# Kernel optimization log

Measured on AMD Instinct MI355X. Metric: run time of the kernel, lower is better.

The kernel has to match this reference:

```python
import jax, jax.numpy as jnp
import numpy as np

B, N, FIN = 32, 1024, 6
KCHEB = 3
CLASS_NUM = 40


def _pairwise_adj(x):
    # x: [B, N, D] -> exp(-squared_euclidean_dist) adjacency [B, N, N]
    inner = jnp.einsum('bnd,bmd->bnm', x, x)
    sq = jnp.sum(x * x, axis=-1)
    d2 = sq[:, :, None] - 2.0 * inner + sq[:, None, :]
    return jnp.exp(-d2)


def _get_laplacian(adj):
    # normalized Laplacian: I - D^{-1/2} A D^{-1/2}
    deg = jnp.sum(adj, axis=-1)                       # [B, N]
    d_is = 1.0 / jnp.sqrt(deg)                        # [B, N]
    eye = jnp.eye(adj.shape[-1], dtype=adj.dtype)
    return eye - d_is[:, :, None] * adj * d_is[:, None, :]


def _cheb_conv(x, L, W, b):
    # Chebyshev graph conv: sum_k T_k(L) x W_k + b;  W: [K, Fin, Fout]
    x0 = x
    x1 = jnp.einsum('bnm,bmf->bnf', L, x0)
    out = jnp.einsum('bnf,fg->bng', x0, W[0]) + jnp.einsum('bnf,fg->bng', x1, W[1])
    xk_2, xk_1 = x0, x1
    for k in range(2, W.shape[0]):
        xk = 2.0 * jnp.einsum('bnm,bmf->bnf', L, xk_1) - xk_2
        out = out + jnp.einsum('bnf,fg->bng', xk, W[k])
        xk_2, xk_1 = xk_1, xk
    return out + b


def setup_inputs() -> dict:
    key = jax.random.key(0)
    ks = jax.random.split(key, 16)

    def w(k, shape, fan_in):
        return jax.random.normal(k, shape, dtype=jnp.float32) / np.sqrt(fan_in)

    return {
        'x': jax.random.normal(ks[0], (B, N, FIN), dtype=jnp.float32),
        'W1': w(ks[1], (KCHEB, 6, 128), 6 * KCHEB),
        'b1': jnp.zeros((128,), jnp.float32),
        'W2': w(ks[2], (KCHEB, 128, 512), 128 * KCHEB),
        'b2': jnp.zeros((512,), jnp.float32),
        'W3': w(ks[3], (KCHEB, 512, 1024), 512 * KCHEB),
        'b3': jnp.zeros((1024,), jnp.float32),
        'fc1_w': w(ks[4], (1024, 512), 1024),
        'fc1_b': jnp.zeros((512,), jnp.float32),
        'fc2_w': w(ks[5], (512, 128), 512),
        'fc2_b': jnp.zeros((128,), jnp.float32),
        'fc3_w': w(ks[6], (128, CLASS_NUM), 128),
        'fc3_b': jnp.zeros((CLASS_NUM,), jnp.float32),
    }


def reference(x, W1, b1, W2, b2, W3, b3, fc1_w, fc1_b, fc2_w, fc2_b, fc3_w, fc3_b):
    # Laplacians are computed under torch.no_grad in the original
    L = _get_laplacian(_pairwise_adj(x))
    out = jax.nn.relu(_cheb_conv(x, L, W1, b1))        # [B, N, 128]

    L = _get_laplacian(_pairwise_adj(out))
    out = jax.nn.relu(_cheb_conv(out, L, W2, b2))      # [B, N, 512]

    L = _get_laplacian(_pairwise_adj(out))
    out = jax.nn.relu(_cheb_conv(out, L, W3, b3))      # [B, N, 1024]

    out = jnp.max(out, axis=1)                          # global max pool -> [B, 1024]
    out = jax.nn.relu(out @ fc1_w + fc1_b)              # dropout is identity at eval
    out = jax.nn.relu(out @ fc2_w + fc2_b)
    out = out @ fc3_w + fc3_b                           # [B, CLASS_NUM]
    return out
```

## Files before the change

kernel.cpp:

```cpp
#include <hip/hip_runtime.h>
#include <cstddef>


#define NN 1024

typedef unsigned short ushort_t;
typedef __bf16 bf16x8 __attribute__((ext_vector_type(8)));
typedef float f32x4 __attribute__((ext_vector_type(4)));

__device__ inline ushort_t f2bf(float f) {
    unsigned int u = __float_as_uint(f);
    u = (u + 0x7fffu + ((u >> 16) & 1u)) >> 16;
    return (ushort_t)u;
}
__device__ inline float bf2f(ushort_t s) {
    return __uint_as_float(((unsigned int)s) << 16);
}

__device__ __attribute__((always_inline)) inline void gld16(
    const ushort_t* g, ushort_t* l) {
    __builtin_amdgcn_global_load_lds(
        (__attribute__((address_space(1))) void*)(ushort_t*)g,
        (__attribute__((address_space(3))) void*)l, 16, 0, 0);
}

__global__ void zero_kernel(float* __restrict__ p, int n) {
    int i = blockIdx.x * blockDim.x + threadIdx.x;
    if (i < n) p[i] = 0.f;
}

__global__ __launch_bounds__(256) void wconvT_kernel(
    const float* __restrict__ W, ushort_t* __restrict__ Wt, int Fi, int Fo, int Ks) {
    int p = blockIdx.z;
    int k0 = blockIdx.y * 64, g0 = blockIdx.x * 64;
    __shared__ float T[64][65];
    int t = threadIdx.x;
#pragma unroll
    for (int q = 0; q < 16; ++q) {
        int kr = (t >> 6) + 4 * q, gc = t & 63;
        int k = k0 + kr, g = g0 + gc;
        T[kr][gc] = (k < Fi && g < Fo) ? W[((size_t)p * Fi + k) * Fo + g] : 0.f;
    }
    __syncthreads();
#pragma unroll
    for (int q = 0; q < 16; ++q) {
        int gr = (t >> 6) + 4 * q, kc = t & 63;
        int g = g0 + gr, k = k0 + kc;
        if (g < Fo && k < Ks)
            Wt[((size_t)p * Fo + g) * Ks + k] = f2bf(T[kc][gr]);
    }
}

__global__ __launch_bounds__(256) void prep2_kernel(
    const float* __restrict__ X, ushort_t* __restrict__ hi, ushort_t* __restrict__ lo,
    ushort_t* __restrict__ Xt, float* __restrict__ sq, int F, int Fp, int bsh) {
    int L = blockIdx.x;
    int b = L & ((1 << bsh) - 1), n0 = (L >> bsh) * 64;
    int t = threadIdx.x;
    __shared__ float T[64][65];
    __shared__ float red[4][64];
    const float* Xb = X + ((size_t)b * NN + n0) * F;
    float sacc = 0.f;

    for (int f0 = 0; f0 < Fp; f0 += 64) {
        __syncthreads();
#pragma unroll
        for (int p = 0; p < 16; ++p) {
            int nr = (t >> 6) + 4 * p, fc = t & 63;
            int f = f0 + fc;
            T[nr][fc] = (f < F) ? Xb[(size_t)nr * F + f] : 0.f;
        }
        __syncthreads();
#pragma unroll
        for (int p = 0; p < 16; ++p) {
            int nr = (t >> 6) + 4 * p, fc = t & 63;
            int f = f0 + fc;
            if (f < Fp) {
                float x = T[nr][fc];
                ushort_t h = f2bf(x);
                size_t off = ((size_t)b * NN + n0 + nr) * Fp + f;
                hi[off] = h;
                lo[off] = f2bf(x - bf2f(h));
            }
        }
#pragma unroll
        for (int p = 0; p < 16; ++p) {
            int fr = (t >> 6) + 4 * p;
            int f = f0 + fr;
            if (f < F)
                Xt[((size_t)b * Fp + f) * NN + n0 + (t & 63)] = f2bf(T[t & 63][fr]);
        }
        {
            int nl = t & 63, fq = t >> 6;
#pragma unroll
            for (int fc = 0; fc < 16; ++fc) {
                float v = T[nl][fq * 16 + fc];
                sacc += v * v;
            }
        }
    }
    red[t >> 6][t & 63] = sacc;
    __syncthreads();
    if (t < 64)
        sq[(size_t)b * NN + n0 + t] = red[0][t] + red[1][t] + red[2][t] + red[3][t];
}

__global__ __launch_bounds__(256) void adj_kernel(
    const ushort_t* __restrict__ hi, const ushort_t* __restrict__ lo,
    const float* __restrict__ sq, ushort_t* __restrict__ Abf,
    float* __restrict__ deg_part, int Fp, int bsh, int BCv) {
    int t = threadIdx.x;
    int L = blockIdx.x;
    int b = L & ((1 << bsh) - 1);
    int rest = L >> bsh;
    int m0 = (rest & 7) * 128, n0 = (rest >> 3) * 128;
    const ushort_t* Hb = hi + (size_t)b * NN * Fp;
    const ushort_t* Lb = lo + (size_t)b * NN * Fp;
    ushort_t* Ab = Abf + (size_t)b * NN * NN;
    const float* sqb = sq + (size_t)b * NN;

    int lane = t & 63, quad = lane >> 4, l16 = lane & 15, wave = t >> 6;
    int rowoff = (wave >> 1) * 64, coloff = (wave & 1) * 64;

    __shared__ __align__(16) ushort_t smem[40960];

    f32x4 acc[4][4];
#pragma unroll
    for (int i = 0; i < 4; ++i)
#pragma unroll
        for (int j = 0; j < 4; ++j) acc[i][j] = (f32x4){0.f, 0.f, 0.f, 0.f};

    int rr0 = t >> 2, kq = (t & 3) * 8;
    int rr1 = rr0 + 64;
    const ushort_t* pAh0 = Hb + (size_t)(n0 + rr0) * Fp + kq;
    const ushort_t* pAh1 = Hb + (size_t)(n0 + rr1) * Fp + kq;
    const ushort_t* pAl0 = Lb + (size_t)(n0 + rr0) * Fp + kq;
    const ushort_t* pAl1 = Lb + (size_t)(n0 + rr1) * Fp + kq;
    const ushort_t* pBh0 = Hb + (size_t)(m0 + rr0) * Fp + kq;
    const ushort_t* pBh1 = Hb + (size_t)(m0 + rr1) * Fp + kq;
    const ushort_t* pBl0 = Lb + (size_t)(m0 + rr0) * Fp + kq;
    const ushort_t* pBl1 = Lb + (size_t)(m0 + rr1) * Fp + kq;
    int o0 = rr0 * 40 + kq, o1 = rr1 * 40 + kq;

    {
        *(uint4*)&smem[o0]         = *(const uint4*)pAh0;
        *(uint4*)&smem[o1]         = *(const uint4*)pAh1;
        *(uint4*)&smem[5120 + o0]  = *(const uint4*)pAl0;
        *(uint4*)&smem[5120 + o1]  = *(const uint4*)pAl1;
        *(uint4*)&smem[10240 + o0] = *(const uint4*)pBh0;
        *(uint4*)&smem[10240 + o1] = *(const uint4*)pBh1;
        *(uint4*)&smem[15360 + o0] = *(const uint4*)pBl0;
        *(uint4*)&smem[15360 + o1] = *(const uint4*)pBl1;
    }
    __syncthreads();

    int NIT = Fp >> 5;
    for (int it = 0; it < NIT; ++it) {
        int cur = (it & 1) * 20480;
        int nxt = 20480 - cur;
        uint4 rh0, rh1, rl0, rl1, sh0, sh1, sl0, sl1;
        if (it + 1 < NIT) {
            int k = (it + 1) * 32;
            rh0 = *(const uint4*)(pAh0 + k); rh1 = *(const uint4*)(pAh1 + k);
            rl0 = *(const uint4*)(pAl0 + k); rl1 = *(const uint4*)(pAl1 + k);
            sh0 = *(const uint4*)(pBh0 + k); sh1 = *(const uint4*)(pBh1 + k);
            sl0 = *(const uint4*)(pBl0 + k); sl1 = *(const uint4*)(pBl1 + k);
        }
        ushort_t* Ah = smem + cur;
        ushort_t* Al = smem + cur + 5120;
        ushort_t* Bh = smem + cur + 10240;
        ushort_t* Bl = smem + cur + 15360;
        bf16x8 ah[4], al[4], bh[4], bl[4];
#pragma unroll
        for (int i = 0; i < 4; ++i) {
            ah[i] = *(const bf16x8*)&Ah[(rowoff + i * 16 + l16) * 40 + quad * 8];
            al[i] = *(const bf16x8*)&Al[(rowoff + i * 16 + l16) * 40 + quad * 8];
        }
#pragma unroll
        for (int j = 0; j < 4; ++j) {
            bh[j] = *(const bf16x8*)&Bh[(coloff + j * 16 + l16) * 40 + quad * 8];
            bl[j] = *(const bf16x8*)&Bl[(coloff + j * 16 + l16) * 40 + quad * 8];
        }
#pragma unroll
        for (int i = 0; i < 4; ++i)
#pragma unroll
            for (int j = 0; j < 4; ++j) {
                acc[i][j] = __builtin_amdgcn_mfma_f32_16x16x32_bf16(al[i], bh[j], acc[i][j], 0, 0, 0);
                acc[i][j] = __builtin_amdgcn_mfma_f32_16x16x32_bf16(ah[i], bl[j], acc[i][j], 0, 0, 0);
                acc[i][j] = __builtin_amdgcn_mfma_f32_16x16x32_bf16(ah[i], bh[j], acc[i][j], 0, 0, 0);
            }
        if (it + 1 < NIT) {
            *(uint4*)&smem[nxt + o0]         = rh0;
            *(uint4*)&smem[nxt + o1]         = rh1;
            *(uint4*)&smem[nxt + 5120 + o0]  = rl0;
            *(uint4*)&smem[nxt + 5120 + o1]  = rl1;
            *(uint4*)&smem[nxt + 10240 + o0] = sh0;
            *(uint4*)&smem[nxt + 10240 + o1] = sh1;
            *(uint4*)&smem[nxt + 15360 + o0] = sl0;
            *(uint4*)&smem[nxt + 15360 + o1] = sl1;
        }
        __syncthreads();
    }

    float rs[4][4];
#pragma unroll
    for (int i = 0; i < 4; ++i)
#pragma unroll
        for (int r = 0; r < 4; ++r) rs[i][r] = 0.f;

#pragma unroll
    for (int j = 0; j < 4; ++j) {
        int m = m0 + coloff + j * 16 + l16;
        float sm = sqb[m];
#pragma unroll
        for (int i = 0; i < 4; ++i) {
#pragma unroll
            for (int r = 0; r < 4; ++r) {
                int n = n0 + rowoff + i * 16 + quad * 4 + r;
                float v = __expf(2.f * acc[i][j][r] - sqb[n] - sm);
                Ab[(size_t)n * NN + m] = f2bf(v);
                rs[i][r] += v;
            }
        }
    }
    int slot = (rest & 7) * 2 + (wave & 1);
#pragma unroll
    for (int i = 0; i < 4; ++i)
#pragma unroll
        for (int r = 0; r < 4; ++r) {
            float s = rs[i][r];
            s += __shfl_xor(s, 1);
            s += __shfl_xor(s, 2);
            s += __shfl_xor(s, 4);
            s += __shfl_xor(s, 8);
            if (l16 == 0)
                deg_part[((size_t)slot * BCv + b) * NN + n0 + rowoff + i * 16 + quad * 4 + r] = s;
        }
}

__global__ __launch_bounds__(256) void disscale_kernel(
    ushort_t* __restrict__ Xt, const float* __restrict__ deg_part,
    float* __restrict__ dis, int Fp, int bsh, int BCv) {
    int L = blockIdx.x;
    int b = L & ((1 << bsh) - 1), n0 = (L >> bsh) * 64;
    int t = threadIdx.x;
    __shared__ float dloc[64];
    if (t < 64) {
        float s = 0.f;
#pragma unroll
        for (int k = 0; k < 16; ++k) s += deg_part[((size_t)k * BCv + b) * NN + n0 + t];
        float d = rsqrtf(s);
        dloc[t] = d;
        dis[(size_t)b * NN + n0 + t] = d;
    }
    __syncthreads();
    int lane = t & 63, fq = t >> 6;
    float d = dloc[lane];
    ushort_t* Xb = Xt + (size_t)b * Fp * NN + n0 + lane;
    for (int f = fq; f < Fp; f += 4) {
        size_t off = (size_t)f * NN;
        Xb[off] = f2bf(bf2f(Xb[off]) * d);
    }
}

__global__ __launch_bounds__(256) void lx_kernel(
    const ushort_t* __restrict__ Abf, const float* __restrict__ dis,
    const ushort_t* __restrict__ in_t, const ushort_t* __restrict__ x0t,
    ushort_t* __restrict__ out_t, ushort_t* __restrict__ out_b,
    int F, int Fp, int mode, int ft, int bsh) {
    int t = threadIdx.x;
    int L = blockIdx.x;
    int b = L & ((1 << bsh) - 1);
    int rest = L >> bsh;
    int m0 = (rest % ft) * 128;
    int n0 = (rest / ft) * 64;
    const ushort_t* Ain = in_t + (size_t)b * Fp * NN;
    const ushort_t* Ab = Abf + (size_t)b * NN * NN;

    int lane = t & 63, quad = lane >> 4, l16 = lane & 15, wave = t >> 6;
    int rowoff = wave * 32;

    __shared__ __align__(16) ushort_t smem[18432];

    f32x4 acc[2][4];
#pragma unroll
    for (int i = 0; i < 2; ++i)
#pragma unroll
        for (int j = 0; j < 4; ++j) acc[i][j] = (f32x4){0.f, 0.f, 0.f, 0.f};

    int lr = lane >> 2;
    int lks = (((lane & 3) ^ ((lane >> 3) & 3)) * 8);
    int qsw = ((quad ^ ((l16 >> 1) & 3)) * 8);
    int rbase = wave * 32;
    const ushort_t* gA = Ain + (size_t)(m0 + rbase + lr) * NN + lks;
    const ushort_t* gB = Ab + (size_t)(n0 + wave * 16 + lr) * NN + lks;

#define LX_STAGE(BOFF, CI)                                            \
    {                                                                 \
        int k_ = (CI) * 32;                                           \
        ushort_t* As_ = smem + (BOFF);                                \
        gld16(gA + k_, As_ + rbase * 32);                             \
        gld16(gA + (size_t)16 * NN + k_, As_ + rbase * 32 + 512);     \
        gld16(gB + k_, As_ + 4096 + wave * 16 * 32);                  \
    }
#define LX_COMP(BOFF)                                                            \
    {                                                                            \
        ushort_t* As_ = smem + (BOFF);                                           \
        ushort_t* Bs_ = As_ + 4096;                                              \
        bf16x8 af[2], bfv[4];                                                    \
        _Pragma("unroll")                                                        \
        for (int i = 0; i < 2; ++i)                                              \
            af[i] = *(const bf16x8*)&As_[(rowoff + i * 16 + l16) * 32 + qsw];    \
        _Pragma("unroll")                                                        \
        for (int j = 0; j < 4; ++j)                                              \
            bfv[j] = *(const bf16x8*)&Bs_[(j * 16 + l16) * 32 + qsw];            \
        _Pragma("unroll")                                                        \
        for (int i = 0; i < 2; ++i)                                              \
            _Pragma("unroll")                                                    \
            for (int j = 0; j < 4; ++j)                                          \
                acc[i][j] = __builtin_amdgcn_mfma_f32_16x16x32_bf16(af[i], bfv[j], acc[i][j], 0, 0, 0); \
    }

    LX_STAGE(0, 0);
    LX_STAGE(6144, 1);
    int cur = 0;
    for (int ci = 0; ci < 32; ++ci) {
        if (ci < 31) { asm volatile("s_waitcnt vmcnt(3)" ::: "memory"); }
        else         { asm volatile("s_waitcnt vmcnt(0)" ::: "memory"); }
        __builtin_amdgcn_s_barrier();
        asm volatile("" ::: "memory");
        if (ci + 2 < 32) {
            int noff = cur + 12288; if (noff >= 18432) noff -= 18432;
            LX_STAGE(noff, ci + 2);
        }
        LX_COMP(cur);
        cur += 6144; if (cur >= 18432) cur = 0;
    }
#undef LX_STAGE
#undef LX_COMP
    __syncthreads();

#pragma unroll
    for (int j = 0; j < 4; ++j) {
        int nl = j * 16 + l16;
        int n = n0 + nl;
        float dn = dis[(size_t)b * NN + n];
        float inv = 1.f / dn;
        float dn2 = dn * dn;
#pragma unroll
        for (int i = 0; i < 2; ++i) {
#pragma unroll
            for (int r = 0; r < 4; ++r) {
                int fl = rowoff + i * 16 + quad * 4 + r;
                int f = m0 + fl;
                float o = 0.f;
                if (f < F) {
                    float a = acc[i][j][r];
                    size_t off = (size_t)f * NN + n;
                    float xin = bf2f(Ain[off]);
                    if (mode == 0) {
                        out_t[(size_t)b * Fp * NN + off] = f2bf(xin - dn2 * a);
                        o = inv * xin - dn * a;
                    } else {
                        float x0 = bf2f(x0t[(size_t)b * Fp * NN + off]);
                        o = inv * (2.f * xin - x0) - 2.f * dn * a;
                    }
                }
                smem[nl * 128 + (((fl >> 3) ^ (nl & 7)) << 3) + (fl & 7)] = f2bf(o);
            }
        }
    }
    __syncthreads();
    for (int s2 = t; s2 < 1024; s2 += 256) {
        int nl = s2 >> 4, oct = s2 & 15;
        int fg = m0 + oct * 8;
        if (fg < Fp) {
            uint4 v = *(const uint4*)&smem[nl * 128 + ((oct ^ (nl & 7)) << 3)];
            *(uint4*)(out_b + ((size_t)b * NN + n0 + nl) * Fp + fg) = v;
        }
    }
}

__global__ __launch_bounds__(256) void proj_kernel(
    const ushort_t* __restrict__ X0, const ushort_t* __restrict__ X1,
    const ushort_t* __restrict__ X2, const ushort_t* __restrict__ Wt,
    const float* __restrict__ bias, float* __restrict__ O, float* __restrict__ pool,
    int Fp, int Fo, int b0, int n_g, int bsh) {
    int t = threadIdx.x;
    int L = blockIdx.x;
    int c = L & ((1 << bsh) - 1);
    int rest = L >> bsh;
    int g0 = (rest % n_g) * 128;
    int r0 = (c * 8 + rest / n_g) * 128;
    int lane = t & 63, quad = lane >> 4, l16 = lane & 15, wave = t >> 6;
    int rowoff = (wave >> 1) * 64, coloff = (wave & 1) * 64;

    __shared__ __align__(16) ushort_t smem[24576];

    f32x4 acc[4][4];
#pragma unroll
    for (int i = 0; i < 4; ++i)
#pragma unroll
        for (int j = 0; j < 4; ++j) acc[i][j] = (f32x4){0.f, 0.f, 0.f, 0.f};

    int lr = lane >> 2;
    int lks = (((lane & 3) ^ ((lane >> 3) & 3)) * 8);
    int qsw = ((quad ^ ((l16 >> 1) & 3)) * 8);
    int rbase = wave * 32;
    int nk = Fp >> 5;
    int NIT = 3 * nk;
    size_t FoFp = (size_t)Fo * Fp;
    size_t r16 = (size_t)16 * Fp;

#define PJ_STAGE(BOFF, CI)                                                    \
    {                                                                         \
        int p_ = (CI) / nk;                                                   \
        int k_ = ((CI) - p_ * nk) * 32 + lks;                                 \
        const ushort_t* Xp_ = (p_ == 0) ? X0 : ((p_ == 1) ? X1 : X2);         \
        const ushort_t* ga_ = Xp_ + (size_t)(r0 + rbase + lr) * Fp + k_;      \
        const ushort_t* gb_ = Wt + (size_t)p_ * FoFp +                        \
                              (size_t)(g0 + rbase + lr) * Fp + k_;            \
        ushort_t* As_ = smem + (BOFF);                                        \
        ushort_t* Bs_ = As_ + 4096;                                           \
        gld16(ga_, As_ + rbase * 32);                                         \
        gld16(ga_ + r16, As_ + rbase * 32 + 512);                             \
        gld16(gb_, Bs_ + rbase * 32);                                         \
        gld16(gb_ + r16, Bs_ + rbase * 32 + 512);                             \
    }
#define PJ_COMP(BOFF)                                                           \
    {                                                                           \
        ushort_t* As_ = smem + (BOFF);                                          \
        ushort_t* Bs_ = As_ + 4096;                                             \
        bf16x8 af[4], bfv[4];                                                   \
        _Pragma("unroll")                                                       \
        for (int i = 0; i < 4; ++i)                                             \
            af[i] = *(const bf16x8*)&As_[(rowoff + i * 16 + l16) * 32 + qsw];   \
        _Pragma("unroll")                                                       \
        for (int j = 0; j < 4; ++j)                                             \
            bfv[j] = *(const bf16x8*)&Bs_[(coloff + j * 16 + l16) * 32 + qsw];  \
        _Pragma("unroll")                                                       \
        for (int i = 0; i < 4; ++i)                                             \
            _Pragma("unroll")                                                   \
            for (int j = 0; j < 4; ++j)                                         \
                acc[i][j] = __builtin_amdgcn_mfma_f32_16x16x32_bf16(af[i], bfv[j], acc[i][j], 0, 0, 0); \
    }

    PJ_STAGE(0, 0);
    PJ_STAGE(8192, 1);
    int cur = 0;
    for (int ci = 0; ci < NIT; ++ci) {
        if (ci < NIT - 1) { asm volatile("s_waitcnt vmcnt(4)" ::: "memory"); }
        else              { asm volatile("s_waitcnt vmcnt(0)" ::: "memory"); }
        __builtin_amdgcn_s_barrier();
        asm volatile("" ::: "memory");
        if (ci + 2 < NIT) {
            int noff = cur + 16384; if (noff >= 24576) noff -= 24576;
            PJ_STAGE(noff, ci + 2);
        }
        PJ_COMP(cur);
        cur += 8192; if (cur >= 24576) cur = 0;
    }
#undef PJ_STAGE
#undef PJ_COMP

    float bias_l[4];
#pragma unroll
    for (int j = 0; j < 4; ++j) bias_l[j] = bias[g0 + coloff + j * 16 + l16];

    if (O) {
#pragma unroll
        for (int i = 0; i < 4; ++i) {
#pragma unroll
            for (int r = 0; r < 4; ++r) {
                int row = r0 + rowoff + i * 16 + quad * 4 + r;
#pragma unroll
                for (int j = 0; j < 4; ++j) {
                    int g = g0 + coloff + j * 16 + l16;
                    O[(size_t)row * Fo + g] = fmaxf(acc[i][j][r] + bias_l[j], 0.f);
                }
            }
        }
    } else {
        float mj[4];
#pragma unroll
        for (int j = 0; j < 4; ++j) {
            float m = 0.f;
#pragma unroll
            for (int i = 0; i < 4; ++i)
#pragma unroll
                for (int r = 0; r < 4; ++r)
                    m = fmaxf(m, acc[i][j][r] + bias_l[j]);
            m = fmaxf(m, 0.f);
            m = fmaxf(m, __shfl_xor(m, 16));
            m = fmaxf(m, __shfl_xor(m, 32));
            mj[j] = m;
        }
        if (quad == 0) {
            int smp = b0 + (r0 >> 10);
#pragma unroll
            for (int j = 0; j < 4; ++j)
                atomicMax((int*)&pool[(size_t)smp * 1024 + g0 + coloff + j * 16 + l16],
                          __float_as_int(mj[j]));
        }
    }
}

__global__ __launch_bounds__(256) void fc_kernel(
    const float* __restrict__ In, const float* __restrict__ W,
    const float* __restrict__ bias, float* __restrict__ out,
    int K, int Nout, int relu) {
    int r = blockIdx.y;
    int c0 = blockIdx.x * 64;
    int t = threadIdx.x;
    int cl = t & 63, ks = t >> 6;
    int c = c0 + cl;
    int kchunk = K >> 2;
    int k0 = ks * kchunk, k1 = k0 + kchunk;
    float s = 0.f;
    if (c < Nout) {
        const float* ip = In + (size_t)r * K;
        const float* wp = W + c;
#pragma unroll 4
        for (int k = k0; k < k1; ++k) s += ip[k] * wp[(size_t)k * Nout];
    }
    __shared__ float red[4][64];
    red[ks][cl] = s;
    __syncthreads();
    if (t < 64 && c0 + t < Nout) {
        float v = red[0][t] + red[1][t] + red[2][t] + red[3][t] + bias[c0 + t];
        if (relu) v = fmaxf(v, 0.f);
        out[(size_t)r * Nout + c0 + t] = v;
    }
}

extern "C" void kernel_launch(void* const* d_in, const int* in_sizes, int n_in,
                              void* d_out, int out_size, void* d_ws, size_t ws_size,
                              hipStream_t stream) {
    const float* x    = (const float*)d_in[0];
    const float* W1   = (const float*)d_in[1];
    const float* b1   = (const float*)d_in[2];
    const float* W2   = (const float*)d_in[3];
    const float* b2   = (const float*)d_in[4];
    const float* W3   = (const float*)d_in[5];
    const float* b3   = (const float*)d_in[6];
    const float* fc1w = (const float*)d_in[7];
    const float* fc1b = (const float*)d_in[8];
    const float* fc2w = (const float*)d_in[9];
    const float* fc2b = (const float*)d_in[10];
    const float* fc3w = (const float*)d_in[11];
    const float* fc3b = (const float*)d_in[12];
    float* out = (float*)d_out;

    auto need = [](size_t BCv) -> size_t {
        size_t us = (size_t)BCv * 1024;
        return 2 * (us * 1024) + 10 * (us * 512) + 2 * 1781760ull +
               4 * (us * 128) + 4 * (us * 512) + 4 * us + 64 * us + 4 * us +
               4 * (32768ull + 16384 + 4096) + 256;
    };
    int BCv = (ws_size >= need(16)) ? 16 : 8;
    int NCH = 32 / BCv;
    int bsh = (BCv == 16) ? 4 : 3;

    size_t usc = (size_t)BCv * 1024;
    size_t Asz = usc * 1024;
    size_t SLv = usc * 512;
    ushort_t* Abf  = (ushort_t*)d_ws;
    ushort_t* X0hi = Abf + Asz;
    ushort_t* X0lo = X0hi + SLv;
    ushort_t* X0t  = X0lo + SLv;
    ushort_t* X1t  = X0t + SLv;
    ushort_t* X1b  = X1t + SLv;
    ushort_t* Wt   = X1b + SLv;
    float* O1   = (float*)(Wt + 1781760);
    float* O2   = O1 + usc * 128;
    float* sq   = O2 + usc * 512;
    float* degp = sq + usc;
    float* dis  = degp + 16 * usc;
    float* pool = dis + usc;
    float* f1   = pool + 32768;
    float* f2   = f1 + 16384;
    ushort_t* X2b = X0lo;

    wconvT_kernel<<<dim3(2, 1, 3), 256, 0, stream>>>(W1, Wt, 6, 128, 32);
    wconvT_kernel<<<dim3(8, 2, 3), 256, 0, stream>>>(W2, Wt + 12288, 128, 512, 128);
    wconvT_kernel<<<dim3(16, 8, 3), 256, 0, stream>>>(W3, Wt + 208896, 512, 1024, 512);
    zero_kernel<<<128, 256, 0, stream>>>(pool, 32768);

    for (int c = 0; c < NCH; ++c) {
        int b0 = c * BCv;
        struct LayerDef {
            const float* X; int F, Fp, Fo;
            const ushort_t* Wtl; const float* bias; float* O;
        };
        LayerDef L[3] = {
            { x + (size_t)b0 * NN * 6, 6,   32,  128,  Wt,          b1, O1 },
            { O1,                      128, 128, 512,  Wt + 12288,  b2, O2 },
            { O2,                      512, 512, 1024, Wt + 208896, b3, nullptr },
        };
        for (int li = 0; li < 3; ++li) {
            LayerDef& Ld = L[li];
            int F = Ld.F, Fp = Ld.Fp;
            int ft = (F + 127) / 128;
            int n_g = Ld.Fo / 128;
            prep2_kernel<<<16 * BCv, 256, 0, stream>>>(Ld.X, X0hi, X0lo, X0t, sq, F, Fp, bsh);
            adj_kernel<<<64 * BCv, 256, 0, stream>>>(X0hi, X0lo, sq, Abf, degp, Fp, bsh, BCv);
            disscale_kernel<<<16 * BCv, 256, 0, stream>>>(X0t, degp, dis, Fp, bsh, BCv);
            lx_kernel<<<ft * 16 * BCv, 256, 0, stream>>>(
                Abf, dis, X0t, nullptr, X1t, X1b, F, Fp, 0, ft, bsh);
            lx_kernel<<<ft * 16 * BCv, 256, 0, stream>>>(
                Abf, dis, X1t, X0t, nullptr, X2b, F, Fp, 1, ft, bsh);
            proj_kernel<<<n_g * 8 * BCv, 256, 0, stream>>>(
                X0hi, X1b, X2b, Ld.Wtl, Ld.bias, Ld.O, pool, Fp, Ld.Fo, b0, n_g, bsh);
        }
    }

    fc_kernel<<<dim3(8, 32), 256, 0, stream>>>(pool, fc1w, fc1b, f1, 1024, 512, 1);
    fc_kernel<<<dim3(2, 32), 256, 0, stream>>>(f1, fc2w, fc2b, f2, 512, 128, 1);
    fc_kernel<<<dim3(1, 32), 256, 0, stream>>>(f2, fc3w, fc3b, out, 128, 40, 0);
}
```

Before: 964.8 us.

## Enlarge proj_kernel tile to 256 rows with 512 threads, drop LDS swizzle

The projection GEMM moves from 256-thread blocks computing 128x128 tiles to 512-thread blocks computing 256x128 tiles. Each block loads twice as many activation rows against the same weight tile, which halves weight traffic per output, and the triple-buffered LDS grows to match. The XOR swizzle on LDS staging and reads is also removed in both lx_kernel and proj_kernel, which simplifies addressing but may bring back LDS bank conflicts on the bf16x8 reads. The larger block raises LDS use per block and may lower occupancy.

```diff
diff --git a/kernel.cpp b/kernel.cpp
--- a/kernel.cpp
+++ b/kernel.cpp
@@ -288,12 +288,10 @@
 #pragma unroll
         for (int j = 0; j < 4; ++j) acc[i][j] = (f32x4){0.f, 0.f, 0.f, 0.f};
 
-    int lr = lane >> 2;
-    int lks = (((lane & 3) ^ ((lane >> 3) & 3)) * 8);
-    int qsw = ((quad ^ ((l16 >> 1) & 3)) * 8);
+    int lr = lane >> 2, lk = (lane & 3) * 8;
     int rbase = wave * 32;
-    const ushort_t* gA = Ain + (size_t)(m0 + rbase + lr) * NN + lks;
-    const ushort_t* gB = Ab + (size_t)(n0 + wave * 16 + lr) * NN + lks;
+    const ushort_t* gA = Ain + (size_t)(m0 + rbase + lr) * NN + lk;
+    const ushort_t* gB = Ab + (size_t)(n0 + wave * 16 + lr) * NN + lk;
 
 #define LX_STAGE(BOFF, CI)                                            \
     {                                                                 \
@@ -310,10 +308,10 @@
         bf16x8 af[2], bfv[4];                                                    \
         _Pragma("unroll")                                                        \
         for (int i = 0; i < 2; ++i)                                              \
-            af[i] = *(const bf16x8*)&As_[(rowoff + i * 16 + l16) * 32 + qsw];    \
+            af[i] = *(const bf16x8*)&As_[(rowoff + i * 16 + l16) * 32 + quad * 8]; \
         _Pragma("unroll")                                                        \
         for (int j = 0; j < 4; ++j)                                              \
-            bfv[j] = *(const bf16x8*)&Bs_[(j * 16 + l16) * 32 + qsw];            \
+            bfv[j] = *(const bf16x8*)&Bs_[(j * 16 + l16) * 32 + quad * 8];       \
         _Pragma("unroll")                                                        \
         for (int i = 0; i < 2; ++i)                                              \
             _Pragma("unroll")                                                    \
@@ -381,7 +379,7 @@
     }
 }
 
-__global__ __launch_bounds__(256) void proj_kernel(
+__global__ __launch_bounds__(512) void proj_kernel(
     const ushort_t* __restrict__ X0, const ushort_t* __restrict__ X1,
     const ushort_t* __restrict__ X2, const ushort_t* __restrict__ Wt,
     const float* __restrict__ bias, float* __restrict__ O, float* __restrict__ pool,
@@ -391,11 +389,11 @@
     int c = L & ((1 << bsh) - 1);
     int rest = L >> bsh;
     int g0 = (rest % n_g) * 128;
-    int r0 = (c * 8 + rest / n_g) * 128;
+    int r0 = (c * 4 + rest / n_g) * 256;
     int lane = t & 63, quad = lane >> 4, l16 = lane & 15, wave = t >> 6;
     int rowoff = (wave >> 1) * 64, coloff = (wave & 1) * 64;
 
-    __shared__ __align__(16) ushort_t smem[24576];
+    __shared__ __align__(16) ushort_t smem[36864];
 
     f32x4 acc[4][4];
 #pragma unroll
@@ -403,10 +401,7 @@
 #pragma unroll
         for (int j = 0; j < 4; ++j) acc[i][j] = (f32x4){0.f, 0.f, 0.f, 0.f};
 
-    int lr = lane >> 2;
-    int lks = (((lane & 3) ^ ((lane >> 3) & 3)) * 8);
-    int qsw = ((quad ^ ((l16 >> 1) & 3)) * 8);
-    int rbase = wave * 32;
+    int lr = lane >> 2, lk = (lane & 3) * 8;
     int nk = Fp >> 5;
     int NIT = 3 * nk;
     size_t FoFp = (size_t)Fo * Fp;
@@ -415,29 +410,28 @@
 #define PJ_STAGE(BOFF, CI)                                                    \
     {                                                                         \
         int p_ = (CI) / nk;                                                   \
-        int k_ = ((CI) - p_ * nk) * 32 + lks;                                 \
+        int k_ = ((CI) - p_ * nk) * 32 + lk;                                  \
         const ushort_t* Xp_ = (p_ == 0) ? X0 : ((p_ == 1) ? X1 : X2);         \
-        const ushort_t* ga_ = Xp_ + (size_t)(r0 + rbase + lr) * Fp + k_;      \
+        const ushort_t* ga_ = Xp_ + (size_t)(r0 + wave * 32 + lr) * Fp + k_;  \
         const ushort_t* gb_ = Wt + (size_t)p_ * FoFp +                        \
-                              (size_t)(g0 + rbase + lr) * Fp + k_;            \
-        ushort_t* As_ = smem + (BOFF);                                        \
-        ushort_t* Bs_ = As_ + 4096;                                           \
-        gld16(ga_, As_ + rbase * 32);                                         \
-        gld16(ga_ + r16, As_ + rbase * 32 + 512);                             \
-        gld16(gb_, Bs_ + rbase * 32);                                         \
-        gld16(gb_ + r16, Bs_ + rbase * 32 + 512);                             \
+                              (size_t)(g0 + wave * 16 + lr) * Fp + k_;        \
+        ushort_t* As_ = smem + (BOFF) + wave * 1024;                          \
+        ushort_t* Bs_ = smem + (BOFF) + 8192 + wave * 512;                    \
+        gld16(ga_, As_);                                                      \
+        gld16(ga_ + r16, As_ + 512);                                          \
+        gld16(gb_, Bs_);                                                      \
     }
 #define PJ_COMP(BOFF)                                                           \
     {                                                                           \
         ushort_t* As_ = smem + (BOFF);                                          \
-        ushort_t* Bs_ = As_ + 4096;                                             \
+        ushort_t* Bs_ = As_ + 8192;                                             \
         bf16x8 af[4], bfv[4];                                                   \
         _Pragma("unroll")                                                       \
         for (int i = 0; i < 4; ++i)                                             \
-            af[i] = *(const bf16x8*)&As_[(rowoff + i * 16 + l16) * 32 + qsw];   \
+            af[i] = *(const bf16x8*)&As_[(rowoff + i * 16 + l16) * 32 + quad * 8];  \
         _Pragma("unroll")                                                       \
         for (int j = 0; j < 4; ++j)                                             \
-            bfv[j] = *(const bf16x8*)&Bs_[(coloff + j * 16 + l16) * 32 + qsw];  \
+            bfv[j] = *(const bf16x8*)&Bs_[(coloff + j * 16 + l16) * 32 + quad * 8]; \
         _Pragma("unroll")                                                       \
         for (int i = 0; i < 4; ++i)                                             \
             _Pragma("unroll")                                                   \
@@ -446,19 +440,19 @@
     }
 
     PJ_STAGE(0, 0);
-    PJ_STAGE(8192, 1);
+    PJ_STAGE(12288, 1);
     int cur = 0;
     for (int ci = 0; ci < NIT; ++ci) {
-        if (ci < NIT - 1) { asm volatile("s_waitcnt vmcnt(4)" ::: "memory"); }
+        if (ci < NIT - 1) { asm volatile("s_waitcnt vmcnt(3)" ::: "memory"); }
         else              { asm volatile("s_waitcnt vmcnt(0)" ::: "memory"); }
         __builtin_amdgcn_s_barrier();
         asm volatile("" ::: "memory");
         if (ci + 2 < NIT) {
-            int noff = cur + 16384; if (noff >= 24576) noff -= 24576;
+            int noff = cur + 24576; if (noff >= 36864) noff -= 36864;
             PJ_STAGE(noff, ci + 2);
         }
         PJ_COMP(cur);
-        cur += 8192; if (cur >= 24576) cur = 0;
+        cur += 12288; if (cur >= 36864) cur = 0;
     }
 #undef PJ_STAGE
 #undef PJ_COMP
@@ -609,7 +603,7 @@
                 Abf, dis, X0t, nullptr, X1t, X1b, F, Fp, 0, ft, bsh);
             lx_kernel<<<ft * 16 * BCv, 256, 0, stream>>>(
                 Abf, dis, X1t, X0t, nullptr, X2b, F, Fp, 1, ft, bsh);
-            proj_kernel<<<n_g * 8 * BCv, 256, 0, stream>>>(
+            proj_kernel<<<n_g * 4 * BCv, 512, 0, stream>>>(
                 X0hi, X1b, X2b, Ld.Wtl, Ld.bias, Ld.O, pool, Fp, Ld.Fo, b0, n_g, bsh);
         }
     }
```

New measurement: 968.9 us. Within noise of the previous version (+0.4%).
